# Kernel tuning notes

Hardware: AMD Instinct MI355X
Metric: run time of the kernel (lower is better)

Reference implementation:

```python
import jax, jax.numpy as jnp
import numpy as np

N_NODES = 20000
N_EDGES = 640000
C_IN = 128      # num_node_features
K_FOLDS = 8     # num_edge_features
FILTERS = 128


def setup_inputs() -> dict:
    key = jax.random.key(0)
    k1, k2, k3, k4, k5, k6 = jax.random.split(key, 6)
    node_features = jax.random.normal(k1, (N_NODES, C_IN), dtype=jnp.float32)
    edge_features = jax.random.uniform(k2, (K_FOLDS, N_EDGES), dtype=jnp.float32)
    rows = jax.random.randint(k3, (N_EDGES,), 0, N_NODES)
    cols = jax.random.randint(k4, (N_EDGES,), 0, N_NODES)
    indices = jnp.stack([rows, cols], axis=1).astype(jnp.int64)
    # glorot_uniform kernel [K, C_in, filters]
    limit = np.sqrt(6.0 / (C_IN + FILTERS))
    kernel = jax.random.uniform(k5, (K_FOLDS, C_IN, FILTERS), dtype=jnp.float32,
                                minval=-limit, maxval=limit)
    bias = jnp.zeros((FILTERS,), dtype=jnp.float32)
    return {
        "node_features": node_features,
        "edge_features": edge_features,
        "kernel": kernel,
        "bias": bias,
        "indices": indices,
        "out_size": N_NODES,
    }


def reference(node_features, edge_features, kernel, bias, indices, out_size):
    # fold_conv: out[i,f] = sum_{e: row(e)=i} sum_k ef[k,e] * (x[col(e)] @ kernel[k])[f]
    row = indices[:, 0]
    col = indices[:, 1]
    xg = node_features[col]  # [E, C] gathered source-node features
    E = xg.shape[0]
    msgs = jnp.zeros((E, kernel.shape[2]), dtype=node_features.dtype)
    # Loop over the small fixed number of folds (K=8); each iteration is a
    # dense [E,C]x[C,F] matmul scaled by the per-edge fold weight.
    for k in range(kernel.shape[0]):
        msgs = msgs + (xg @ kernel[k]) * edge_features[k][:, None]
    out = jax.ops.segment_sum(msgs, row, num_segments=out_size)  # [out_size, F]
    out = out + bias  # bias_add; activation is None (linear)
    return out
```

## Files before the change

### kernel.cpp

```cpp
#include <hip/hip_runtime.h>
#include <cstddef>
#include <cstdint>

static constexpr int kNodes   = 20000;
static constexpr int kEdges   = 640000;
static constexpr int kCin     = 128;
static constexpr int kFolds   = 8;
static constexpr int kFilters = 128;
static constexpr int kKdim    = kFolds * kCin;
static constexpr int kCap     = 80;

static constexpr int kNBucketF = 1250;
static constexpr int kCapF     = 768;
static constexpr int kBin1Blk  = 80;

typedef __attribute__((ext_vector_type(8))) short v8s;
typedef __attribute__((ext_vector_type(4))) float v4f;

__device__ __forceinline__ unsigned short f2bf(float f) {
    union { float f; uint32_t u; } v; v.f = f;
    const uint32_t u = v.u;
    return (unsigned short)((u + 0x7fffu + ((u >> 16) & 1u)) >> 16);
}
__device__ __forceinline__ float bf2f(unsigned short s) {
    union { uint32_t u; float f; } v; v.u = ((uint32_t)s) << 16;
    return v.f;
}

__global__ __launch_bounds__(256) void prep_k(
    const int2*  __restrict__ idx2,
    const float* __restrict__ ef,
    const float* __restrict__ x,
    const float* __restrict__ W,
    int* __restrict__ bucketCnt,
    int2* __restrict__ pairs,
    unsigned int* __restrict__ rec,
    unsigned short* __restrict__ xb,
    unsigned short* __restrict__ Wp)
{
    const int b = blockIdx.x;
    const int t = threadIdx.x;
    if (b < 2500) {
        const int e = b * 256 + t;
        const int2 rc = idx2[e];
        union { uint4 q; unsigned int w[4]; unsigned short s[8]; } o;
        #pragma unroll
        for (int k = 0; k < kFolds; ++k)
            o.s[k] = f2bf(ef[(size_t)k * kEdges + e]);
        uint4* recp = (uint4*)(rec + (size_t)e * 8);
        recp[0] = make_uint4((unsigned)rc.y, o.w[0], o.w[1], o.w[2]);
        recp[1] = make_uint4(o.w[3], 0u, 0u, 0u);
    } else if (b < 3750) {
        const int i = (b - 2500) * 2048 + t * 8;
        const float4 a = *(const float4*)(x + i);
        const float4 c = *(const float4*)(x + i + 4);
        union { uint4 q; unsigned short s[8]; } o;
        o.s[0] = f2bf(a.x); o.s[1] = f2bf(a.y); o.s[2] = f2bf(a.z); o.s[3] = f2bf(a.w);
        o.s[4] = f2bf(c.x); o.s[5] = f2bf(c.y); o.s[6] = f2bf(c.z); o.s[7] = f2bf(c.w);
        *(uint4*)(xb + i) = o.q;
    } else if (b < 3814) {
        const int t2 = (b - 3750) * 256 + t;
        const int n  = t2 & 127;
        const int k8 = t2 >> 7;
        const int c  = k8 >> 2;
        const int q  = k8 & 3;
        union { uint4 qv; unsigned short s[8]; } o;
        #pragma unroll
        for (int j = 0; j < 8; ++j)
            o.s[j] = f2bf(W[(size_t)(k8 * 8 + j) * kFilters + n]);
        *(uint4*)(Wp + (((size_t)c * kFilters + n) * 4 + q) * 8) = o.qv;
    } else {
        __shared__ int hist[kNBucketF];
        __shared__ int base[kNBucketF];
        const int bb = b - 3814;
        const int e0 = bb * 8192;

        for (int i = t; i < kNBucketF; i += 256) hist[i] = 0;
        __syncthreads();

        #pragma unroll 4
        for (int i = 0; i < 32; ++i) {
            const int e = e0 + i * 256 + t;
            if (e < kEdges)
                atomicAdd(&hist[idx2[e].x >> 4], 1);
        }
        __syncthreads();

        for (int i = t; i < kNBucketF; i += 256) {
            const int h = hist[i];
            base[i] = h ? atomicAdd(&bucketCnt[i], h) : 0;
            hist[i] = 0;
        }
        __syncthreads();

        #pragma unroll 4
        for (int i = 0; i < 32; ++i) {
            const int e = e0 + i * 256 + t;
            if (e < kEdges) {
                const int row = idx2[e].x;
                const int bk  = row >> 4;
                const int sl  = base[bk] + atomicAdd(&hist[bk], 1);
                if (sl < kCapF)
                    pairs[(size_t)bk * kCapF + sl] = make_int2(row, e);
            }
        }
    }
}

static constexpr int kSWS2 = 1048;

__global__ __launch_bounds__(256) void pull_k(
    const unsigned short* __restrict__ xb,
    const int2* __restrict__ pairs,
    const int*  __restrict__ bucketCnt,
    const unsigned int* __restrict__ rec,
    const unsigned short* __restrict__ Wp,
    const float* __restrict__ bias,
    float* __restrict__ out)
{
    __shared__ int sCol[16][kCap + 4];
    __shared__ int sDeg[16];
    __shared__ int sCnt[16];
    __shared__ __align__(16) char arena[16 * (kCap + 4) * 8 * 4];

    float (*sEf)[kCap + 4][8] = (float(*)[kCap + 4][8])arena;
    unsigned short (*sS)[kSWS2] = (unsigned short(*)[kSWS2])arena;

    const int t  = threadIdx.x;
    const int B  = blockIdx.x;
    const int n0 = B * 16;

    if (t < 16) sCnt[t] = 0;
    __syncthreads();
    {
        int nseg = bucketCnt[B];
        nseg = nseg < kCapF ? nseg : kCapF;
        const int2* seg = pairs + (size_t)B * kCapF;
        for (int s = t; s < nseg; s += 256) {
            const int2 p = seg[s];
            const int rl = p.x & 15;
            const int c  = atomicAdd(&sCnt[rl], 1);
            if (c < kCap) sCol[rl][c] = p.y;
        }
    }
    __syncthreads();

    {
        const int g16 = t >> 4;
        const int s0  = t & 15;
        int dg = sCnt[g16];
        dg = dg < kCap ? dg : kCap;
        for (int s = s0; s < dg; s += 16) {
            const int e = sCol[g16][s];
            const uint4 q0    = *(const uint4*)(rec + (size_t)e * 8);
            const unsigned w3 = rec[(size_t)e * 8 + 4];
            sCol[g16][s] = (int)q0.x;
            sEf[g16][s][0] = bf2f((unsigned short)(q0.y));
            sEf[g16][s][1] = bf2f((unsigned short)(q0.y >> 16));
            sEf[g16][s][2] = bf2f((unsigned short)(q0.z));
            sEf[g16][s][3] = bf2f((unsigned short)(q0.z >> 16));
            sEf[g16][s][4] = bf2f((unsigned short)(q0.w));
            sEf[g16][s][5] = bf2f((unsigned short)(q0.w >> 16));
            sEf[g16][s][6] = bf2f((unsigned short)(w3));
            sEf[g16][s][7] = bf2f((unsigned short)(w3 >> 16));
        }
        const int dgP = (dg + 3) & ~3;
        for (int s = dg + s0; s < dgP; s += 16) {
            sCol[g16][s] = 0;
            #pragma unroll
            for (int k = 0; k < kFolds; ++k) sEf[g16][s][k] = 0.f;
        }
        if (s0 == 0) sDeg[g16] = dg;
    }
    __syncthreads();

    const int wave = t >> 6;
    const int lane = t & 63;
    const int g    = lane >> 4;
    const int c8   = (lane & 15) * 8;
    const int ln   = wave * 4 + g;
    const int degP = (sDeg[ln] + 3) & ~3;

    float acc[8][8];
    #pragma unroll
    for (int k = 0; k < 8; ++k)
        #pragma unroll
        for (int j = 0; j < 8; ++j) acc[k][j] = 0.f;

    const unsigned short* xbase = xb + c8;

    auto proc = [&](v8s xv, int i) {
        float xf[8];
        #pragma unroll
        for (int jj = 0; jj < 8; ++jj) xf[jj] = bf2f((unsigned short)xv[jj]);
        const float4 wa = *(const float4*)&sEf[ln][i][0];
        const float4 wc = *(const float4*)&sEf[ln][i][4];
        const float w[8] = {wa.x, wa.y, wa.z, wa.w, wc.x, wc.y, wc.z, wc.w};
        #pragma unroll
        for (int k = 0; k < 8; ++k)
            #pragma unroll
            for (int jj = 0; jj < 8; ++jj)
                acc[k][jj] += w[k] * xf[jj];
    };

    v8s x0 = (v8s)0, x1 = (v8s)0, x2 = (v8s)0, x3 = (v8s)0;
    if (degP > 0) {
        x0 = *(const v8s*)(xbase + (size_t)sCol[ln][0] * kCin);
        x1 = *(const v8s*)(xbase + (size_t)sCol[ln][1] * kCin);
        x2 = *(const v8s*)(xbase + (size_t)sCol[ln][2] * kCin);
        x3 = *(const v8s*)(xbase + (size_t)sCol[ln][3] * kCin);
    }

    for (int i = 0; i < degP; i += 4) {
        const int j = (i + 4 < degP) ? (i + 4) : i;
        const v8s y0 = *(const v8s*)(xbase + (size_t)sCol[ln][j]     * kCin);
        const v8s y1 = *(const v8s*)(xbase + (size_t)sCol[ln][j + 1] * kCin);
        const v8s y2 = *(const v8s*)(xbase + (size_t)sCol[ln][j + 2] * kCin);
        const v8s y3 = *(const v8s*)(xbase + (size_t)sCol[ln][j + 3] * kCin);

        proc(x0, i); proc(x1, i + 1); proc(x2, i + 2); proc(x3, i + 3);

        x0 = y0; x1 = y1; x2 = y2; x3 = y3;
    }

    __syncthreads();
    #pragma unroll
    for (int k = 0; k < 8; ++k) {
        union { uint4 q; unsigned short s[8]; } o;
        #pragma unroll
        for (int j = 0; j < 8; ++j) o.s[j] = f2bf(acc[k][j]);
        *(uint4*)&sS[ln][k * kCin + c8] = o.q;
    }
    __syncthreads();

    const int quad = lane >> 4;
    const int r16  = lane & 15;

    v4f acc2[2];
    acc2[0] = (v4f){0.f, 0.f, 0.f, 0.f};
    acc2[1] = (v4f){0.f, 0.f, 0.f, 0.f};

    const unsigned short* wb0 = Wp + (((size_t)(wave * 32 + r16)) * 4 + quad) * 8;
    const unsigned short* wb1 = wb0 + 16 * 4 * 8;

    #pragma unroll 4
    for (int c = 0; c < 32; ++c) {
        const v8s a  = *(const v8s*)&sS[r16][c * 32 + quad * 8];
        const v8s b0 = *(const v8s*)(wb0 + (size_t)c * kFilters * 32);
        const v8s b1 = *(const v8s*)(wb1 + (size_t)c * kFilters * 32);
        acc2[0] = __builtin_amdgcn_mfma_f32_16x16x32_bf16(a, b0, acc2[0], 0, 0, 0);
        acc2[1] = __builtin_amdgcn_mfma_f32_16x16x32_bf16(a, b1, acc2[1], 0, 0, 0);
    }

    #pragma unroll
    for (int i = 0; i < 2; ++i) {
        const int n  = (wave * 2 + i) * 16 + r16;
        const float bv = bias[n];
        #pragma unroll
        for (int r = 0; r < 4; ++r) {
            const int m = n0 + quad * 4 + r;
            out[(size_t)m * kFilters + n] = acc2[i][r] + bv;
        }
    }
}

extern "C" void kernel_launch(void* const* d_in, const int* in_sizes, int n_in,
                              void* d_out, int out_size, void* d_ws, size_t ws_size,
                              hipStream_t stream) {
    const float* x    = (const float*)d_in[0];
    const float* ef   = (const float*)d_in[1];
    const float* W    = (const float*)d_in[2];
    const float* bias = (const float*)d_in[3];
    const int2*  idx2 = (const int2*)d_in[4];
    float* out = (float*)d_out;

    char* ws = (char*)d_ws;
    int2*           pairs  = (int2*)(ws);
    int*            bucketCnt = (int*)(ws + 7680000);
    unsigned int*   rec    = (unsigned int*)(ws + 40960000);
    unsigned short* xb     = (unsigned short*)(ws + 67840000);
    unsigned short* Wp     = (unsigned short*)(ws + 72960000);

    hipMemsetAsync(bucketCnt, 0, kNBucketF * sizeof(int), stream);

    prep_k<<<3814 + kBin1Blk, 256, 0, stream>>>(idx2, ef, x, W, bucketCnt,
                                                pairs, rec, xb, Wp);
    pull_k<<<kNodes / 16, 256, 0, stream>>>(xb, pairs, bucketCnt, rec,
                                            Wp, bias, out);
}
```

Before: 168.2 us.

## Launch edge binning blocks first, cache rows in registers, pack pairs to 32 bits

After: 159.5 us. 1.05x faster.

```diff
diff --git a/kernel.cpp b/kernel.cpp
--- a/kernel.cpp
+++ b/kernel.cpp
@@ -33,15 +33,55 @@
     const float* __restrict__ x,
     const float* __restrict__ W,
     int* __restrict__ bucketCnt,
-    int2* __restrict__ pairs,
+    unsigned int* __restrict__ pairs,
     unsigned int* __restrict__ rec,
     unsigned short* __restrict__ xb,
     unsigned short* __restrict__ Wp)
 {
     const int b = blockIdx.x;
     const int t = threadIdx.x;
-    if (b < 2500) {
-        const int e = b * 256 + t;
+    if (b < kBin1Blk) {
+        __shared__ int hist[kNBucketF];
+        __shared__ int base[kNBucketF];
+        const int e0 = b * 8192;
+
+        for (int i = t; i < kNBucketF; i += 256) hist[i] = 0;
+        __syncthreads();
+
+        int rows[32];
+        #pragma unroll
+        for (int i = 0; i < 32; ++i) {
+            const int e = e0 + i * 256 + t;
+            int row = -1;
+            if (e < kEdges) {
+                row = idx2[e].x;
+                atomicAdd(&hist[row >> 4], 1);
+            }
+            rows[i] = row;
+        }
+        __syncthreads();
+
+        for (int i = t; i < kNBucketF; i += 256) {
+            const int h = hist[i];
+            base[i] = h ? atomicAdd(&bucketCnt[i], h) : 0;
+            hist[i] = 0;
+        }
+        __syncthreads();
+
+        #pragma unroll
+        for (int i = 0; i < 32; ++i) {
+            const int row = rows[i];
+            if (row >= 0) {
+                const int e  = e0 + i * 256 + t;
+                const int bk = row >> 4;
+                const int sl = base[bk] + atomicAdd(&hist[bk], 1);
+                if (sl < kCapF)
+                    pairs[(size_t)bk * kCapF + sl] =
+                        ((unsigned)(row & 15) << 24) | (unsigned)e;
+            }
+        }
+    } else if (b < 2580) {
+        const int e = (b - kBin1Blk) * 256 + t;
         const int2 rc = idx2[e];
         union { uint4 q; unsigned int w[4]; unsigned short s[8]; } o;
         #pragma unroll
@@ -50,16 +90,16 @@
         uint4* recp = (uint4*)(rec + (size_t)e * 8);
         recp[0] = make_uint4((unsigned)rc.y, o.w[0], o.w[1], o.w[2]);
         recp[1] = make_uint4(o.w[3], 0u, 0u, 0u);
-    } else if (b < 3750) {
-        const int i = (b - 2500) * 2048 + t * 8;
+    } else if (b < 3830) {
+        const int i = (b - 2580) * 2048 + t * 8;
         const float4 a = *(const float4*)(x + i);
         const float4 c = *(const float4*)(x + i + 4);
         union { uint4 q; unsigned short s[8]; } o;
         o.s[0] = f2bf(a.x); o.s[1] = f2bf(a.y); o.s[2] = f2bf(a.z); o.s[3] = f2bf(a.w);
         o.s[4] = f2bf(c.x); o.s[5] = f2bf(c.y); o.s[6] = f2bf(c.z); o.s[7] = f2bf(c.w);
         *(uint4*)(xb + i) = o.q;
-    } else if (b < 3814) {
-        const int t2 = (b - 3750) * 256 + t;
+    } else {
+        const int t2 = (b - 3830) * 256 + t;
         const int n  = t2 & 127;
         const int k8 = t2 >> 7;
         const int c  = k8 >> 2;
@@ -69,41 +109,6 @@
         for (int j = 0; j < 8; ++j)
             o.s[j] = f2bf(W[(size_t)(k8 * 8 + j) * kFilters + n]);
         *(uint4*)(Wp + (((size_t)c * kFilters + n) * 4 + q) * 8) = o.qv;
-    } else {
-        __shared__ int hist[kNBucketF];
-        __shared__ int base[kNBucketF];
-        const int bb = b - 3814;
-        const int e0 = bb * 8192;
-
-        for (int i = t; i < kNBucketF; i += 256) hist[i] = 0;
-        __syncthreads();
-
-        #pragma unroll 4
-        for (int i = 0; i < 32; ++i) {
-            const int e = e0 + i * 256 + t;
-            if (e < kEdges)
-                atomicAdd(&hist[idx2[e].x >> 4], 1);
-        }
-        __syncthreads();
-
-        for (int i = t; i < kNBucketF; i += 256) {
-            const int h = hist[i];
-            base[i] = h ? atomicAdd(&bucketCnt[i], h) : 0;
-            hist[i] = 0;
-        }
-        __syncthreads();
-
-        #pragma unroll 4
-        for (int i = 0; i < 32; ++i) {
-            const int e = e0 + i * 256 + t;
-            if (e < kEdges) {
-                const int row = idx2[e].x;
-                const int bk  = row >> 4;
-                const int sl  = base[bk] + atomicAdd(&hist[bk], 1);
-                if (sl < kCapF)
-                    pairs[(size_t)bk * kCapF + sl] = make_int2(row, e);
-            }
-        }
     }
 }
 
@@ -111,7 +116,7 @@
 
 __global__ __launch_bounds__(256) void pull_k(
     const unsigned short* __restrict__ xb,
-    const int2* __restrict__ pairs,
+    const unsigned int* __restrict__ pairs,
     const int*  __restrict__ bucketCnt,
     const unsigned int* __restrict__ rec,
     const unsigned short* __restrict__ Wp,
@@ -135,12 +140,12 @@
     {
         int nseg = bucketCnt[B];
         nseg = nseg < kCapF ? nseg : kCapF;
-        const int2* seg = pairs + (size_t)B * kCapF;
+        const unsigned int* seg = pairs + (size_t)B * kCapF;
         for (int s = t; s < nseg; s += 256) {
-            const int2 p = seg[s];
-            const int rl = p.x & 15;
+            const unsigned p = seg[s];
+            const int rl = (int)(p >> 24);
             const int c  = atomicAdd(&sCnt[rl], 1);
-            if (c < kCap) sCol[rl][c] = p.y;
+            if (c < kCap) sCol[rl][c] = (int)(p & 0xFFFFFFu);
         }
     }
     __syncthreads();
@@ -275,16 +280,16 @@
     float* out = (float*)d_out;
 
     char* ws = (char*)d_ws;
-    int2*           pairs  = (int2*)(ws);
-    int*            bucketCnt = (int*)(ws + 7680000);
+    unsigned int*   pairs  = (unsigned int*)(ws);
+    int*            bucketCnt = (int*)(ws + 3840000);
     unsigned int*   rec    = (unsigned int*)(ws + 40960000);
     unsigned short* xb     = (unsigned short*)(ws + 67840000);
     unsigned short* Wp     = (unsigned short*)(ws + 72960000);
 
     hipMemsetAsync(bucketCnt, 0, kNBucketF * sizeof(int), stream);
 
-    prep_k<<<3814 + kBin1Blk, 256, 0, stream>>>(idx2, ef, x, W, bucketCnt,
-                                                pairs, rec, xb, Wp);
+    prep_k<<<3894, 256, 0, stream>>>(idx2, ef, x, W, bucketCnt,
+                                     pairs, rec, xb, Wp);
     pull_k<<<kNodes / 16, 256, 0, stream>>>(xb, pairs, bucketCnt, rec,
                                             Wp, bias, out);
 }
```
